# Kernel tuning notes

Measured on AMD Instinct MI355X. Metric: run time of the kernel, lower is better.

Reference implementation:

```python
import math
import jax, jax.numpy as jnp
import numpy as np

H, D = 16, 128
INNER = H * D
QUERY_DIM = 2048
EPS = 1e-6
NUM_SEQ_SHIFTS = 16
MAX_SEQ_LEN = 2048
CHANNEL_SHIFTS = [1, 2, 4, 8]


def compute_seq_shifts(num_shifts, max_len=2048):
    if num_shifts <= 1:
        return [0]
    half = (num_shifts - 1 + 1) // 2
    max_s = max(max_len // 2, 2)
    if half <= 1:
        positive = [1]
    else:
        positive = sorted(set(max(1, round(math.exp(math.log(max_s) * i / (half - 1)))) for i in range(half)))
        while len(positive) < half:
            new_vals = []
            for i in range(len(positive) - 1):
                mid = (positive[i] + positive[i + 1]) // 2
                if mid not in positive and mid not in new_vals:
                    new_vals.append(mid)
                if len(positive) + len(new_vals) >= half:
                    break
            if not new_vals:
                v = positive[-1] + 1
                while len(positive) + len(new_vals) < half and v <= max_s:
                    new_vals.append(v)
                    v += 1
            positive = sorted(set(positive + new_vals))[:half]
    shifts = [0]
    for s in positive:
        shifts.append(s)
        shifts.append(-s)
    return shifts[:num_shifts]

SEQ_SHIFTS = compute_seq_shifts(NUM_SEQ_SHIFTS, MAX_SEQ_LEN)


def setup_inputs() -> dict:
    key = jax.random.key(0)
    ks = jax.random.split(key, 12)
    s = 0.02
    return {
        "x": jax.random.normal(ks[0], (2, 2048, QUERY_DIM), dtype=jnp.float32),
        "wq": jax.random.normal(ks[1], (INNER, QUERY_DIM), dtype=jnp.float32) * s,
        "bq": jnp.zeros((INNER,), jnp.float32),
        "wk": jax.random.normal(ks[2], (INNER, QUERY_DIM), dtype=jnp.float32) * s,
        "bk": jnp.zeros((INNER,), jnp.float32),
        "wv": jax.random.normal(ks[3], (INNER, QUERY_DIM), dtype=jnp.float32) * s,
        "bv": jnp.zeros((INNER,), jnp.float32),
        "gq": jnp.ones((INNER,), jnp.float32),
        "gk": jnp.ones((INNER,), jnp.float32),
        "w_mix": jax.random.normal(ks[4], (1, 1 + len(CHANNEL_SHIFTS)), dtype=jnp.float32) * 0.4,
        "wo": jax.random.normal(ks[5], (QUERY_DIM, INNER), dtype=jnp.float32) * s,
        "bo": jnp.zeros((QUERY_DIM,), jnp.float32),
    }


def _rmsnorm(x, g, eps=EPS):
    return x * jax.lax.rsqrt(jnp.mean(x * x, axis=-1, keepdims=True) + eps) * g


def reference(x, wq, bq, wk, bk, wv, bv, gq, gk, w_mix, wo, bo):
    B, L, _ = x.shape
    scale = D ** (-0.5)
    q = _rmsnorm(x @ wq.T + bq, gq).reshape(B, L, H, D)
    k = _rmsnorm(x @ wk.T + bk, gk).reshape(B, L, H, D)
    v = (x @ wv.T + bv).reshape(B, L, H, D)
    # rolled gather indices: roll(k, s, axis=1)[l] == k[(l - s) % L]
    shifts = np.asarray(SEQ_SHIFTS)  # [S]
    idx = (np.arange(L)[None, :] - shifts[:, None]) % L  # [S, L]
    k_sh = k[:, idx]  # [B, S, L, H, D]
    v_sh = v[:, idx]  # [B, S, L, H, D]
    # channel-shifted q variants: [base, roll 1, 2, 4, 8] along D
    q_all = jnp.stack([q] + [jnp.roll(q, c, axis=-1) for c in CHANNEL_SHIFTS], axis=0)  # [C, B, L, H, D]
    scores = jnp.einsum('cblhd,bslhd->blhsc', q_all, k_sh) * scale  # [B, L, H, S, C]
    mixed = jnp.einsum('blhsc,c->blhs', scores, w_mix[0])  # score_mix Linear(C,1,bias=False)
    attn = jax.nn.softmax(mixed, axis=-1)  # softmax over shifts
    out = jnp.einsum('blhs,bslhd->blhd', attn, v_sh).reshape(B, L, H * D)
    return out @ wo.T + bo
```

## Files before the change

### kernel.cpp

```cpp
#include <hip/hip_runtime.h>
#include <hip/hip_bf16.h>
#include <stdint.h>

typedef __attribute__((ext_vector_type(8))) short v8s;
typedef __attribute__((ext_vector_type(8))) __bf16 bf16x8;
typedef __attribute__((ext_vector_type(4))) float v4f;

__device__ __forceinline__ unsigned short f2bf(float f) {
  unsigned int u = __float_as_uint(f);
  u += 0x7fff + ((u >> 16) & 1);
  return (unsigned short)(u >> 16);
}
__device__ __forceinline__ float bf2f(unsigned short h) {
  return __uint_as_float(((unsigned int)h) << 16);
}

__device__ __forceinline__ void gload_lds16(const void* g, void* l) {
  __builtin_amdgcn_global_load_lds(
      (const __attribute__((address_space(1))) void*)g,
      (__attribute__((address_space(3))) void*)l,
      16, 0, 0);
}

__global__ void cast_main(const float* __restrict__ x,  const float* __restrict__ wq,
                          const float* __restrict__ wk, const float* __restrict__ wv,
                          const float* __restrict__ wo,
                          unsigned short* __restrict__ xb, unsigned short* __restrict__ wqkvb,
                          unsigned short* __restrict__ wob) {
  const size_t MK = 8388608, NK = 4194304;
  size_t i = ((size_t)blockIdx.x * 256 + threadIdx.x) * 4;
  const float* s; unsigned short* d; size_t off;
  if (i < MK)               { s = x;  d = xb;              off = i; }
  else if (i < MK + NK)     { s = wq; d = wqkvb;           off = i - MK; }
  else if (i < MK + 2 * NK) { s = wk; d = wqkvb + NK;      off = i - MK - NK; }
  else if (i < MK + 3 * NK) { s = wv; d = wqkvb + 2 * NK;  off = i - MK - 2 * NK; }
  else                      { s = wo; d = wob;             off = i - MK - 3 * NK; }
  float4 v = *(const float4*)(s + off);
  ushort4 o;
  o.x = f2bf(v.x); o.y = f2bf(v.y); o.z = f2bf(v.z); o.w = f2bf(v.w);
  *(ushort4*)(d + off) = o;
}

#define BM 128
#define BN 128
#define BK 64

template <int OUT>
__global__ __launch_bounds__(256, 4) void gemm_bt(
    const unsigned short* __restrict__ A,
    const unsigned short* __restrict__ B,
    const float* __restrict__ bias0,
    const float* __restrict__ bias1,
    const float* __restrict__ bias2,
    void* __restrict__ D0, void* __restrict__ D1, void* __restrict__ D2,
    int K, int nbx)
{
  __shared__ __align__(16) unsigned short As[BM * BK];
  __shared__ __align__(16) unsigned short Bs[BN * BK];

  const int tid  = threadIdx.x;
  const int lane = tid & 63;
  const int wid  = tid >> 6;
  const int wr   = wid >> 1, wc = wid & 1;

  const int bid = blockIdx.x;
  const int xcd = bid & 7;
  const int c   = bid >> 3;
  const int bx  = xcd * (nbx >> 3) + (c >> 5);
  const int by  = c & 31;
  const int tm  = by * BM;
  const int tn  = bx * BN;

  const int srow = lane >> 3;
  const int scb  = lane & 7;
  const int gco  = (scb ^ srow) * 8;

  v4f acc[4][4];
#pragma unroll
  for (int m = 0; m < 4; ++m)
#pragma unroll
    for (int n = 0; n < 4; ++n)
      acc[m][n] = (v4f){0.f, 0.f, 0.f, 0.f};

  const unsigned short* Ab = A + (size_t)tm * K;
  const unsigned short* Bb = B + (size_t)tn * K;
  const int kTiles = K / BK;

  for (int kt = 0; kt < kTiles; ++kt) {
    const int k0 = kt * BK;
#pragma unroll
    for (int i = 0; i < 4; ++i) {
      const int r0 = wid * 32 + i * 8;
      gload_lds16(Ab + (size_t)(r0 + srow) * K + k0 + gco, &As[r0 * BK]);
    }
#pragma unroll
    for (int i = 0; i < 4; ++i) {
      const int r0 = wid * 32 + i * 8;
      gload_lds16(Bb + (size_t)(r0 + srow) * K + k0 + gco, &Bs[r0 * BK]);
    }
    __syncthreads();

#pragma unroll
    for (int ks = 0; ks < 2; ++ks) {
      bf16x8 av[4], bv[4];
#pragma unroll
      for (int m = 0; m < 4; ++m) {
        const int row  = wr * 64 + m * 16 + (lane & 15);
        const int cl   = ks * 4 + (lane >> 4);
        av[m] = *(const bf16x8*)&As[row * BK + ((cl ^ (row & 7)) * 8)];
      }
#pragma unroll
      for (int n = 0; n < 4; ++n) {
        const int row  = wc * 64 + n * 16 + (lane & 15);
        const int cl   = ks * 4 + (lane >> 4);
        bv[n] = *(const bf16x8*)&Bs[row * BK + ((cl ^ (row & 7)) * 8)];
      }
#pragma unroll
      for (int m = 0; m < 4; ++m)
#pragma unroll
        for (int n = 0; n < 4; ++n)
          acc[m][n] = __builtin_amdgcn_mfma_f32_16x16x32_bf16(av[m], bv[n], acc[m][n], 0, 0, 0);
    }
    __syncthreads();
  }

  const int cr0 = tm + wr * 64 + (lane >> 4) * 4;
  const int cc0 = tn + wc * 64 + (lane & 15);

  if (OUT == 0) {
    float* Dp = (float*)D0;
#pragma unroll
    for (int n = 0; n < 4; ++n) {
      const int col = cc0 + n * 16;
      const float bz = bias0[col];
#pragma unroll
      for (int m = 0; m < 4; ++m) {
#pragma unroll
        for (int r = 0; r < 4; ++r) {
          const int rr = cr0 + m * 16 + r;
          Dp[(size_t)rr * 2048 + col] = acc[m][n][r] + bz;
        }
      }
    }
  } else {
    const int sid = tn >> 11;
    const float* bp = (sid == 0) ? bias0 : (sid == 1) ? bias1 : bias2;
    unsigned short* Dq = (unsigned short*)((sid == 0) ? D0 : (sid == 1) ? D1 : D2);
#pragma unroll
    for (int n = 0; n < 4; ++n) {
      const int col = cc0 + n * 16;
      const int c2 = col & 2047;
      const float bz = bp[c2];
#pragma unroll
      for (int m = 0; m < 4; ++m) {
#pragma unroll
        for (int r = 0; r < 4; ++r) {
          const int rr = cr0 + m * 16 + r;
          const float val = acc[m][n][r] + bz;
          if (sid < 2) {
            Dq[(size_t)rr * 2048 + c2] = f2bf(val);
          } else {
            const int bb = rr >> 11, ll = rr & 2047;
            const int hh = c2 >> 7, dd = c2 & 127;
            Dq[(((size_t)(bb * 16 + hh)) * 2048 + ll) * 128 + dd] = f2bf(val);
          }
        }
      }
    }
  }
}

__global__ __launch_bounds__(256) void rmsnorm_mix(
    const unsigned short* __restrict__ Qb, const unsigned short* __restrict__ Kb,
    unsigned short* __restrict__ Qt, unsigned short* __restrict__ Kt,
    const float* __restrict__ gq, const float* __restrict__ gk,
    const float* __restrict__ wmix)
{
  const int row = blockIdx.x;
  const bool isQ = (blockIdx.y == 0);
  const unsigned short* src = (isQ ? Qb : Kb) + (size_t)row * 2048;
  unsigned short* dstbase = isQ ? Qt : Kt;
  const float* g = isQ ? gq : gk;
  const int b = row >> 11, l = row & 2047;

  __shared__ float sv[2048];
  __shared__ float red[4];

  const int t = threadIdx.x;
  v8s raw = *(const v8s*)(src + t * 8);
  float x[8];
  float ss = 0.f;
#pragma unroll
  for (int j = 0; j < 8; ++j) { x[j] = bf2f((unsigned short)raw[j]); ss += x[j] * x[j]; }
#pragma unroll
  for (int o = 32; o > 0; o >>= 1) ss += __shfl_xor(ss, o, 64);
  if ((t & 63) == 0) red[t >> 6] = ss;
  __syncthreads();
  const float tot = red[0] + red[1] + red[2] + red[3];
  const float inv = rsqrtf(tot * (1.0f / 2048.0f) + 1e-6f);

  const int h = t >> 4;
  unsigned short* dst = dstbase + (((size_t)(b * 16 + h)) * 2048 + l) * 128 + ((t * 8) & 127);

  if (isQ) {
#pragma unroll
    for (int j = 0; j < 8; ++j) sv[t * 8 + j] = x[j] * inv * g[t * 8 + j];
    __syncthreads();
    const float scale = 0.08838834764831845f;
    const float w0 = wmix[0], w1 = wmix[1], w2 = wmix[2], w3 = wmix[3], w4 = wmix[4];
    v8s ov;
#pragma unroll
    for (int j = 0; j < 8; ++j) {
      const int idx = t * 8 + j;
      const int hb = idx & ~127;
      const int d  = idx & 127;
      float a = w0 * sv[hb + d]
              + w1 * sv[hb + ((d - 1) & 127)]
              + w2 * sv[hb + ((d - 2) & 127)]
              + w3 * sv[hb + ((d - 4) & 127)]
              + w4 * sv[hb + ((d - 8) & 127)];
      ov[j] = (short)f2bf(a * scale);
    }
    *(v8s*)dst = ov;
  } else {
    v8s ov;
#pragma unroll
    for (int j = 0; j < 8; ++j) ov[j] = (short)f2bf(x[j] * inv * g[t * 8 + j]);
    *(v8s*)dst = ov;
  }
}

__global__ __launch_bounds__(512, 1) void attention_k(
    const unsigned short* __restrict__ Qt,
    const unsigned short* __restrict__ Kt,
    const unsigned short* __restrict__ Vt,
    unsigned short* __restrict__ AO)
{
  const int bid   = blockIdx.x;
  const int plane = bid & 31;
  const int ch    = bid >> 5;
  const int b = plane >> 4, h = plane & 15;
  const int l0 = ch * 128;
  const int w0 = (l0 + 2048 - 64) & 2047;

  __shared__ __align__(16) unsigned short Ks[256 * 128];
  __shared__ __align__(16) unsigned short Vs[256 * 128];
  __shared__ float sc[128][17];

  const int t    = threadIdx.x;
  const int lane = t & 63;
  const int w    = t >> 6;
  const int li   = t >> 2;
  const int q    = t & 3;
  const int myl  = l0 + li;

  const size_t pbase = (size_t)plane * (2048 * 128);

  {
    const int lr4 = lane >> 4;
    const int cp  = lane & 15;
#pragma unroll
    for (int j = 0; j < 8; ++j) {
      const int seg = w * 8 + j;
      const int rl  = seg * 4 + lr4;
      const int cl  = cp ^ (rl & 7);
      const int g   = (w0 + rl) & 2047;
      gload_lds16(Kt + pbase + (size_t)g * 128 + cl * 8, &Ks[seg * 512]);
      gload_lds16(Vt + pbase + (size_t)g * 128 + cl * 8, &Vs[seg * 512]);
    }
  }

  float qf[32];
  {
    const unsigned short* qp = Qt + pbase + (size_t)myl * 128 + q * 32;
#pragma unroll
    for (int i = 0; i < 4; ++i) {
      v8s qv = *(const v8s*)(qp + i * 8);
#pragma unroll
      for (int j = 0; j < 8; ++j) qf[i * 8 + j] = bf2f((unsigned short)qv[j]);
    }
  }

  asm volatile("s_waitcnt vmcnt(0)" ::: "memory");
  __syncthreads();

  const int SH[16] = {0, 1, -1, 3, -3, 7, -7, 20, -20, 53, -53, 141, -141, 380, -380, 1024};

#pragma unroll
  for (int s = 0; s < 16; ++s) {
    float dot = 0.f;
    if (s < 11) {
      const int rl = li + 64 - SH[s];
#pragma unroll
      for (int i = 0; i < 4; ++i) {
        v8s kv = *(const v8s*)&Ks[rl * 128 + (((q * 4 + i) ^ (rl & 7)) * 8)];
#pragma unroll
        for (int j = 0; j < 8; ++j) dot += qf[i * 8 + j] * bf2f((unsigned short)kv[j]);
      }
    } else {
      const int row = (myl - SH[s]) & 2047;
      const unsigned short* kp = Kt + pbase + (size_t)row * 128 + q * 32;
#pragma unroll
      for (int i = 0; i < 4; ++i) {
        v8s kv = *(const v8s*)(kp + i * 8);
#pragma unroll
        for (int j = 0; j < 8; ++j) dot += qf[i * 8 + j] * bf2f((unsigned short)kv[j]);
      }
    }
    dot += __shfl_xor(dot, 1, 64);
    dot += __shfl_xor(dot, 2, 64);
    if (q == 0) sc[li][s] = dot;
  }
  __syncthreads();

  {
    float v0[16];
#pragma unroll
    for (int s = 0; s < 16; ++s) v0[s] = sc[li][s];
    float mx = v0[0];
#pragma unroll
    for (int s = 1; s < 16; ++s) mx = fmaxf(mx, v0[s]);
    float sum = 0.f;
    float e[4];
#pragma unroll
    for (int s = 0; s < 16; ++s) {
      const float ee = __expf(v0[s] - mx);
      sum += ee;
      if ((s >> 2) == q) e[s & 3] = ee;
    }
    const float inv = 1.f / sum;
    __syncthreads();
#pragma unroll
    for (int i = 0; i < 4; ++i) sc[li][q * 4 + i] = e[i] * inv;
  }
  __syncthreads();

  float o[32];
#pragma unroll
  for (int i = 0; i < 32; ++i) o[i] = 0.f;
#pragma unroll
  for (int s = 0; s < 16; ++s) {
    const float p = sc[li][s];
    if (s < 11) {
      const int rl = li + 64 - SH[s];
#pragma unroll
      for (int i = 0; i < 4; ++i) {
        v8s vv = *(const v8s*)&Vs[rl * 128 + (((q * 4 + i) ^ (rl & 7)) * 8)];
#pragma unroll
        for (int j = 0; j < 8; ++j) o[i * 8 + j] += p * bf2f((unsigned short)vv[j]);
      }
    } else {
      const int row = (myl - SH[s]) & 2047;
      const unsigned short* vp = Vt + pbase + (size_t)row * 128 + q * 32;
#pragma unroll
      for (int i = 0; i < 4; ++i) {
        v8s vv = *(const v8s*)(vp + i * 8);
#pragma unroll
        for (int j = 0; j < 8; ++j) o[i * 8 + j] += p * bf2f((unsigned short)vv[j]);
      }
    }
  }

  unsigned short* op = AO + ((size_t)(b * 2048 + myl)) * 2048 + h * 128 + q * 32;
#pragma unroll
  for (int i = 0; i < 4; ++i) {
    v8s ov;
#pragma unroll
    for (int j = 0; j < 8; ++j) ov[j] = (short)f2bf(o[i * 8 + j]);
    *(v8s*)(op + i * 8) = ov;
  }
}

extern "C" void kernel_launch(void* const* d_in, const int* in_sizes, int n_in,
                              void* d_out, int out_size, void* d_ws, size_t ws_size,
                              hipStream_t stream) {
  const float* x    = (const float*)d_in[0];
  const float* wq   = (const float*)d_in[1];
  const float* bq   = (const float*)d_in[2];
  const float* wk   = (const float*)d_in[3];
  const float* bk   = (const float*)d_in[4];
  const float* wv   = (const float*)d_in[5];
  const float* bv   = (const float*)d_in[6];
  const float* gq   = (const float*)d_in[7];
  const float* gk   = (const float*)d_in[8];
  const float* wmix = (const float*)d_in[9];
  const float* wo   = (const float*)d_in[10];
  const float* bo   = (const float*)d_in[11];

  const int M = 4096;
  const int K = 2048;
  const size_t MB = 1024 * 1024;

  char* ws = (char*)d_ws;
  unsigned short* xb    = (unsigned short*)(ws + 0 * MB);
  unsigned short* Ktr   = (unsigned short*)(ws + 0 * MB);
  unsigned short* wqkvb = (unsigned short*)(ws + 16 * MB);
  unsigned short* Qb    = (unsigned short*)(ws + 40 * MB);
  unsigned short* AOb   = (unsigned short*)(ws + 40 * MB);
  unsigned short* Kb    = (unsigned short*)(ws + 56 * MB);
  unsigned short* Vt    = (unsigned short*)(ws + 72 * MB);
  unsigned short* Qtr   = (unsigned short*)(ws + 88 * MB);
  unsigned short* wob   = (unsigned short*)(ws + 104 * MB);

  cast_main<<<24576, 256, 0, stream>>>(x, wq, wk, wv, wo, xb, wqkvb, wob);

  gemm_bt<1><<<1536, 256, 0, stream>>>(xb, wqkvb, bq, bk, bv, Qb, Kb, Vt, K, 48);

  rmsnorm_mix<<<dim3(M, 2), 256, 0, stream>>>(Qb, Kb, Qtr, Ktr, gq, gk, wmix);
  attention_k<<<512, 512, 0, stream>>>(Qtr, Ktr, Vt, AOb);

  gemm_bt<0><<<512, 256, 0, stream>>>(AOb, wob, bo, nullptr, nullptr, d_out, nullptr, nullptr, K, 16);
}
```

Before: 237.7 us.

## Stage V tile through LDS for coalesced head-major stores; drop XCD block remap

The V-projection epilogue now writes the 128x128 bf16 tile into shared memory, then copies it to the head-major Vt layout with 16-byte vector stores instead of scattered 2-byte stores. The XCD-aware block index swizzle is replaced by a plain 2D grid, and launch bounds drop the minimum blocks per CU from 4 to 2. These changes aim to cut uncoalesced write traffic, at the cost of an extra barrier. They may also lose the L2 locality the swizzle provided and change register allocation.

```diff
diff --git a/kernel.cpp b/kernel.cpp
--- a/kernel.cpp
+++ b/kernel.cpp
@@ -46,30 +46,26 @@
 #define BK 64
 
 template <int OUT>
-__global__ __launch_bounds__(256, 4) void gemm_bt(
+__global__ __launch_bounds__(256, 2) void gemm_bt(
     const unsigned short* __restrict__ A,
     const unsigned short* __restrict__ B,
     const float* __restrict__ bias0,
     const float* __restrict__ bias1,
     const float* __restrict__ bias2,
     void* __restrict__ D0, void* __restrict__ D1, void* __restrict__ D2,
-    int K, int nbx)
+    int K)
 {
-  __shared__ __align__(16) unsigned short As[BM * BK];
-  __shared__ __align__(16) unsigned short Bs[BN * BK];
+  __shared__ __align__(16) unsigned short Sh[2 * BM * BK];
+  unsigned short* As = Sh;
+  unsigned short* Bs = Sh + BM * BK;
 
   const int tid  = threadIdx.x;
   const int lane = tid & 63;
   const int wid  = tid >> 6;
   const int wr   = wid >> 1, wc = wid & 1;
 
-  const int bid = blockIdx.x;
-  const int xcd = bid & 7;
-  const int c   = bid >> 3;
-  const int bx  = xcd * (nbx >> 3) + (c >> 5);
-  const int by  = c & 31;
-  const int tm  = by * BM;
-  const int tn  = bx * BN;
+  const int tm = blockIdx.y * BM;
+  const int tn = blockIdx.x * BN;
 
   const int srow = lane >> 3;
   const int scb  = lane & 7;
@@ -146,25 +142,44 @@
     const int sid = tn >> 11;
     const float* bp = (sid == 0) ? bias0 : (sid == 1) ? bias1 : bias2;
     unsigned short* Dq = (unsigned short*)((sid == 0) ? D0 : (sid == 1) ? D1 : D2);
-#pragma unroll
-    for (int n = 0; n < 4; ++n) {
-      const int col = cc0 + n * 16;
-      const int c2 = col & 2047;
-      const float bz = bp[c2];
-#pragma unroll
-      for (int m = 0; m < 4; ++m) {
-#pragma unroll
-        for (int r = 0; r < 4; ++r) {
-          const int rr = cr0 + m * 16 + r;
-          const float val = acc[m][n][r] + bz;
-          if (sid < 2) {
-            Dq[(size_t)rr * 2048 + c2] = f2bf(val);
-          } else {
-            const int bb = rr >> 11, ll = rr & 2047;
-            const int hh = c2 >> 7, dd = c2 & 127;
-            Dq[(((size_t)(bb * 16 + hh)) * 2048 + ll) * 128 + dd] = f2bf(val);
+    if (sid < 2) {
+#pragma unroll
+      for (int n = 0; n < 4; ++n) {
+        const int col = cc0 + n * 16;
+        const int c2 = col & 2047;
+        const float bz = bp[c2];
+#pragma unroll
+        for (int m = 0; m < 4; ++m) {
+#pragma unroll
+          for (int r = 0; r < 4; ++r) {
+            const int rr = cr0 + m * 16 + r;
+            Dq[(size_t)rr * 2048 + c2] = f2bf(acc[m][n][r] + bz);
           }
         }
+      }
+    } else {
+      const int rl0 = wr * 64 + (lane >> 4) * 4;
+      const int clb = wc * 64 + (lane & 15);
+#pragma unroll
+      for (int n = 0; n < 4; ++n) {
+        const int cl = clb + n * 16;
+        const float bz = bp[(tn & 2047) + cl];
+#pragma unroll
+        for (int m = 0; m < 4; ++m) {
+#pragma unroll
+          for (int r = 0; r < 4; ++r) {
+            Sh[(rl0 + m * 16 + r) * 128 + cl] = f2bf(acc[m][n][r] + bz);
+          }
+        }
+      }
+      __syncthreads();
+      const int bb = tm >> 11, ll0 = tm & 2047;
+      const int hh = (tn & 2047) >> 7;
+      unsigned short* dst = Dq + (((size_t)(bb * 16 + hh)) * 2048 + ll0) * 128;
+#pragma unroll
+      for (int it = 0; it < 8; ++it) {
+        const int off = (it * 256 + tid) * 8;
+        *(v8s*)(dst + off) = *(const v8s*)&Sh[off];
       }
     }
   }
@@ -404,10 +419,10 @@
 
   cast_main<<<24576, 256, 0, stream>>>(x, wq, wk, wv, wo, xb, wqkvb, wob);
 
-  gemm_bt<1><<<1536, 256, 0, stream>>>(xb, wqkvb, bq, bk, bv, Qb, Kb, Vt, K, 48);
+  gemm_bt<1><<<dim3(48, 32), 256, 0, stream>>>(xb, wqkvb, bq, bk, bv, Qb, Kb, Vt, K);
 
   rmsnorm_mix<<<dim3(M, 2), 256, 0, stream>>>(Qb, Kb, Qtr, Ktr, gq, gk, wmix);
   attention_k<<<512, 512, 0, stream>>>(Qtr, Ktr, Vt, AOb);
 
-  gemm_bt<0><<<512, 256, 0, stream>>>(AOb, wob, bo, nullptr, nullptr, d_out, nullptr, nullptr, K, 16);
-}
+  gemm_bt<0><<<dim3(16, 32), 256, 0, stream>>>(AOb, wob, bo, nullptr, nullptr, d_out, nullptr, nullptr, K);
+}
```

After: 221.4 us. -6.9%, faster.
